# Kernel optimization log

Hardware: AMD Instinct MI355X
Metric: run time of the kernel (lower is better)

Reference implementation:

```python
import jax, jax.numpy as jnp
import numpy as np

H = 16
D_MODEL = 1024
D_K = D_MODEL // H
B, S = 4, 2048


def setup_inputs() -> dict:
    key = jax.random.key(0)
    ks = jax.random.split(key, 12)
    s = 1.0 / np.sqrt(D_MODEL)
    inp = {
        "q": jax.random.normal(ks[0], (B, S, D_MODEL), jnp.float32),
        "k": jax.random.normal(ks[1], (B, S, D_MODEL), jnp.float32),
        "v": jax.random.normal(ks[2], (B, S, D_MODEL), jnp.float32),
        "mask": jnp.ones((B, S, S), jnp.int32),
        "Wq": jax.random.normal(ks[3], (D_MODEL, D_MODEL), jnp.float32) * s,
        "bq": jnp.zeros((D_MODEL,), jnp.float32),
        "Wk": jax.random.normal(ks[4], (D_MODEL, D_MODEL), jnp.float32) * s,
        "bk": jnp.zeros((D_MODEL,), jnp.float32),
        "Wv": jax.random.normal(ks[5], (D_MODEL, D_MODEL), jnp.float32) * s,
        "bv": jnp.zeros((D_MODEL,), jnp.float32),
        "Wo": jax.random.normal(ks[6], (D_MODEL, D_MODEL), jnp.float32) * s,
        "bo": jnp.zeros((D_MODEL,), jnp.float32),
    }
    return inp


def _shape_heads(x):
    # [B, S, d_model] -> [B, H, S, d_k]
    b, s, _ = x.shape
    return x.reshape(b, s, H, D_K).transpose(0, 2, 1, 3)


def reference(q, k, v, mask, Wq, bq, Wk, bk, Wv, bv, Wo, bo):
    qh = _shape_heads(q @ Wq + bq)  # [B,H,S,dk]
    kh = _shape_heads(k @ Wk + bk)
    vh = _shape_heads(v @ Wv + bv)
    scores = jnp.einsum("bhqd,bhkd->bhqk", qh, kh) / jnp.sqrt(jnp.float32(D_K))
    scores = jnp.where(mask[:, None, :, :] == 0, jnp.float32(-1e9), scores)
    attn = jax.nn.softmax(scores, axis=-1)  # dropout = identity (eval)
    ctx = jnp.einsum("bhqk,bhkd->bhqd", attn, vh)
    concat = ctx.transpose(0, 2, 1, 3).reshape(q.shape[0], -1, D_MODEL)
    output = concat @ Wo + bo
    return output, attn
```

## Files before the change

### kernel.cpp

```cpp
#include <hip/hip_runtime.h>

#define NH     16
#define SEQ    2048
#define DMODEL 1024
#define DK     64
#define NB     4

typedef __attribute__((ext_vector_type(8))) short short8v;
typedef __attribute__((ext_vector_type(4))) short short4v;
typedef __attribute__((ext_vector_type(4))) float f32x4;

#define EXP_SC 0.18033688011f

__device__ __forceinline__ short f2bf(float x) {
  unsigned u = __float_as_uint(x);
  unsigned r = (u + 0x7FFFu + ((u >> 16) & 1u)) >> 16;
  return (short)r;
}
__device__ __forceinline__ float bf2f(short b) {
  return __uint_as_float(((unsigned)(unsigned short)b) << 16);
}

typedef const __attribute__((address_space(1))) unsigned int* gas_t;
typedef __attribute__((address_space(3))) unsigned int* las_t;
__device__ __forceinline__ void glds16(const void* g, void* l) {
  __builtin_amdgcn_global_load_lds((gas_t)g, (las_t)l, 16, 0, 0);
}

__device__ __forceinline__ void stage_tile(const void* grow0, int gpitchB,
                                           void* ltile, int wid, int lane) {
#pragma unroll
  for (int i = 0; i < 2; ++i) {
    const int row = i * 32 + wid * 8 + (lane >> 3);
    const int srccol = ((lane & 7) * 16) ^ ((lane >> 3) << 4);
    const char* src = reinterpret_cast<const char*>(grow0) + (size_t)row * gpitchB + srccol;
    char* dst = reinterpret_cast<char*>(ltile) + i * 4096 + wid * 1024;
    glds16(src, dst);
  }
}

__device__ __forceinline__ void stage_tile_h8(const void* grow0, int gpitchB,
                                              void* ltile, int wid, int lane) {
  const int row = wid * 8 + (lane >> 3);
  const int srccol = ((lane & 7) * 16) ^ ((lane >> 3) << 4);
  const char* src = reinterpret_cast<const char*>(grow0) + (size_t)row * gpitchB + srccol;
  char* dst = reinterpret_cast<char*>(ltile) + wid * 1024;
  glds16(src, dst);
}
__device__ __forceinline__ void stage_tile128(const void* grow0, int gpitchB,
                                              void* ltile, int wid, int lane) {
#pragma unroll
  for (int i = 0; i < 2; ++i) {
    const int row = i * 64 + wid * 8 + (lane >> 3);
    const int srccol = ((lane & 7) * 16) ^ ((lane >> 3) << 4);
    const char* src = reinterpret_cast<const char*>(grow0) + (size_t)row * gpitchB + srccol;
    char* dst = reinterpret_cast<char*>(ltile) + i * 8192 + wid * 1024;
    glds16(src, dst);
  }
}

__device__ __forceinline__ short8v ldfrag(const short* base, int row, int colByte) {
  return *reinterpret_cast<const short8v*>(
      reinterpret_cast<const char*>(base) + row * 128 + (colByte ^ ((row & 7) << 4)));
}
__device__ __forceinline__ void st8b(short* base, int row, int colByte, short4v v) {
  *reinterpret_cast<short4v*>(
      reinterpret_cast<char*>(base) + row * 128 + (colByte ^ ((row & 7) << 4))) = v;
}

__device__ __forceinline__ void stPf4(float* base, int row, int colByte, float4 v) {
  *reinterpret_cast<float4*>(
      reinterpret_cast<char*>(base) + row * 256 + (colByte ^ ((row & 7) << 4))) = v;
}
__device__ __forceinline__ float4 ldPf4(const float* base, int row, int colByte) {
  return *reinterpret_cast<const float4*>(
      reinterpret_cast<const char*>(base) + row * 256 + (colByte ^ ((row & 7) << 4)));
}

__global__ __launch_bounds__(256) void pack_mask_kernel(
    const int* __restrict__ mask, unsigned long long* __restrict__ bits)
{
  const int t = threadIdx.x;
  const size_t chunk = (size_t)blockIdx.x * 4 + (t >> 6);
  const int lane = t & 63;
  const int m = mask[chunk * 64 + lane];
  const unsigned long long b = __ballot(m != 0);
  if (lane == 0) bits[chunk] = b;
}

__global__ __launch_bounds__(256) void convert_f32_bf16_kernel(
    const float* __restrict__ in, short* __restrict__ out)
{
  const int idx = blockIdx.x * 256 + threadIdx.x;
  const float4 x0 = *reinterpret_cast<const float4*>(&in[(size_t)idx * 8]);
  const float4 x1 = *reinterpret_cast<const float4*>(&in[(size_t)idx * 8 + 4]);
  short8v o;
  o[0] = f2bf(x0.x); o[1] = f2bf(x0.y); o[2] = f2bf(x0.z); o[3] = f2bf(x0.w);
  o[4] = f2bf(x1.x); o[5] = f2bf(x1.y); o[6] = f2bf(x1.z); o[7] = f2bf(x1.w);
  *reinterpret_cast<short8v*>(&out[(size_t)idx * 8]) = o;
}

__global__ __launch_bounds__(256) void transpose_w_all_kernel(
    const float* __restrict__ W0, const float* __restrict__ W1,
    const float* __restrict__ W2, const float* __restrict__ W3,
    short* __restrict__ WT0, short* __restrict__ WT1,
    short* __restrict__ WT2, short* __restrict__ WT3h, short* __restrict__ WT3l)
{
  __shared__ short Th[64][80];
  __shared__ short Tl[64][80];
  const int t  = threadIdx.x;
  const int k0 = blockIdx.x * 64;
  const int n0 = blockIdx.y * 64;
  const int z  = blockIdx.z;
  const float* W = (z == 0) ? W0 : (z == 1) ? W1 : (z == 2) ? W2 : W3;

  const int kl = t >> 2, nc = (t & 3) * 16;
  if (z < 3) {
#pragma unroll
    for (int i = 0; i < 4; ++i) {
      const float4 x = *reinterpret_cast<const float4*>(&W[(size_t)(k0 + kl) * DMODEL + n0 + nc + i * 4]);
      Th[nc + i * 4 + 0][kl] = f2bf(x.x);
      Th[nc + i * 4 + 1][kl] = f2bf(x.y);
      Th[nc + i * 4 + 2][kl] = f2bf(x.z);
      Th[nc + i * 4 + 3][kl] = f2bf(x.w);
    }
    __syncthreads();
    short* WT = (z == 0) ? WT0 : (z == 1) ? WT1 : WT2;
    const int nl = t >> 2, kc = (t & 3) * 16;
#pragma unroll
    for (int i = 0; i < 2; ++i) {
      const short8v y = *reinterpret_cast<const short8v*>(&Th[nl][kc + i * 8]);
      *reinterpret_cast<short8v*>(&WT[(size_t)(n0 + nl) * DMODEL + k0 + kc + i * 8]) = y;
    }
  } else {
#pragma unroll
    for (int i = 0; i < 4; ++i) {
      const float4 x = *reinterpret_cast<const float4*>(&W[(size_t)(k0 + kl) * DMODEL + n0 + nc + i * 4]);
      const float xv[4] = {x.x, x.y, x.z, x.w};
#pragma unroll
      for (int j = 0; j < 4; ++j) {
        const short hi = f2bf(xv[j]);
        const short lo = f2bf(xv[j] - bf2f(hi));
        Th[nc + i * 4 + j][kl] = hi;
        Tl[nc + i * 4 + j][kl] = lo;
      }
    }
    __syncthreads();
    const int nl = t >> 2, kc = (t & 3) * 16;
#pragma unroll
    for (int i = 0; i < 2; ++i) {
      const short8v yh = *reinterpret_cast<const short8v*>(&Th[nl][kc + i * 8]);
      const short8v yl = *reinterpret_cast<const short8v*>(&Tl[nl][kc + i * 8]);
      *reinterpret_cast<short8v*>(&WT3h[(size_t)(n0 + nl) * DMODEL + k0 + kc + i * 8]) = yh;
      *reinterpret_cast<short8v*>(&WT3l[(size_t)(n0 + nl) * DMODEL + k0 + kc + i * 8]) = yl;
    }
  }
}

__global__ __launch_bounds__(256) void proj_mfma_kernel(
    const short* __restrict__ A,
    const short* __restrict__ BT,
    const float* __restrict__ bias,
    short* __restrict__ out)
{
  __shared__ short As[128 * 64];
  __shared__ short Bs[128 * 64];

  const int t = threadIdx.x, lane = t & 63, wid = t >> 6;
  const int g = lane >> 4, r15 = lane & 15;
  const int lid = (blockIdx.x & 7) * 64 + (blockIdx.x >> 3);
  const int m0 = (lid >> 3) * 128, n0 = (lid & 7) * 128;
  const int wm = (wid >> 1) * 64, wn = (wid & 1) * 64;

  f32x4 acc[4][4];
#pragma unroll
  for (int i = 0; i < 4; ++i)
#pragma unroll
    for (int j = 0; j < 4; ++j) acc[i][j] = (f32x4){0.f, 0.f, 0.f, 0.f};

  for (int k0 = 0; k0 < DMODEL; k0 += 64) {
    __syncthreads();
    stage_tile(A + (size_t)m0 * DMODEL + k0, DMODEL * 2, As, wid, lane);
    stage_tile(A + (size_t)(m0 + 64) * DMODEL + k0, DMODEL * 2, As + 64 * 64, wid, lane);
    stage_tile(BT + (size_t)n0 * DMODEL + k0, DMODEL * 2, Bs, wid, lane);
    stage_tile(BT + (size_t)(n0 + 64) * DMODEL + k0, DMODEL * 2, Bs + 64 * 64, wid, lane);
    __syncthreads();

#pragma unroll
    for (int w = 0; w < 2; ++w) {
      short8v a[4], b[4];
#pragma unroll
      for (int i = 0; i < 4; ++i) a[i] = ldfrag(As, wm + i * 16 + r15, w * 64 + g * 16);
#pragma unroll
      for (int j = 0; j < 4; ++j) b[j] = ldfrag(Bs, wn + j * 16 + r15, w * 64 + g * 16);
#pragma unroll
      for (int i = 0; i < 4; ++i)
#pragma unroll
        for (int j = 0; j < 4; ++j)
          acc[i][j] = __builtin_amdgcn_mfma_f32_16x16x32_bf16(a[i], b[j], acc[i][j], 0, 0, 0);
    }
  }

#pragma unroll
  for (int j = 0; j < 4; ++j) {
    const int n = n0 + wn + j * 16 + r15;
    const int hh = n >> 6, dd = n & 63;
    const float bv = bias[n];
#pragma unroll
    for (int i = 0; i < 4; ++i) {
#pragma unroll
      for (int reg = 0; reg < 4; ++reg) {
        const int m = m0 + wm + i * 16 + g * 4 + reg;
        const int bb = m >> 11, ss = m & 2047;
        out[((size_t)(bb * NH + hh) * SEQ + ss) * DK + dd] = f2bf(acc[i][j][reg] + bv);
      }
    }
  }
}

__global__ __launch_bounds__(256) void outproj_mfma_kernel(
    const short* __restrict__ Ahp, const short* __restrict__ Alp,
    const short* __restrict__ BTh, const short* __restrict__ BTl,
    const float* __restrict__ bias, float* __restrict__ out)
{
  __shared__ short Ah[128 * 64];
  __shared__ short Al[128 * 64];
  __shared__ short Bh[128 * 64];
  __shared__ short Bl[128 * 64];

  const int t = threadIdx.x, lane = t & 63, wid = t >> 6;
  const int g = lane >> 4, r15 = lane & 15;
  const int lid = (blockIdx.x & 7) * 64 + (blockIdx.x >> 3);
  const int m0 = (lid >> 3) * 128, n0 = (lid & 7) * 128;
  const int wm = (wid >> 1) * 64, wn = (wid & 1) * 64;

  f32x4 acc[4][4];
#pragma unroll
  for (int i = 0; i < 4; ++i)
#pragma unroll
    for (int j = 0; j < 4; ++j) acc[i][j] = (f32x4){0.f, 0.f, 0.f, 0.f};

  for (int k0 = 0; k0 < DMODEL; k0 += 64) {
    __syncthreads();
    stage_tile(Ahp + (size_t)m0 * DMODEL + k0, DMODEL * 2, Ah, wid, lane);
    stage_tile(Ahp + (size_t)(m0 + 64) * DMODEL + k0, DMODEL * 2, Ah + 64 * 64, wid, lane);
    stage_tile(Alp + (size_t)m0 * DMODEL + k0, DMODEL * 2, Al, wid, lane);
    stage_tile(Alp + (size_t)(m0 + 64) * DMODEL + k0, DMODEL * 2, Al + 64 * 64, wid, lane);
    stage_tile(BTh + (size_t)n0 * DMODEL + k0, DMODEL * 2, Bh, wid, lane);
    stage_tile(BTh + (size_t)(n0 + 64) * DMODEL + k0, DMODEL * 2, Bh + 64 * 64, wid, lane);
    stage_tile(BTl + (size_t)n0 * DMODEL + k0, DMODEL * 2, Bl, wid, lane);
    stage_tile(BTl + (size_t)(n0 + 64) * DMODEL + k0, DMODEL * 2, Bl + 64 * 64, wid, lane);
    __syncthreads();

#pragma unroll
    for (int w = 0; w < 2; ++w) {
      short8v ah[4], al[4];
#pragma unroll
      for (int i = 0; i < 4; ++i) {
        ah[i] = ldfrag(Ah, wm + i * 16 + r15, w * 64 + g * 16);
        al[i] = ldfrag(Al, wm + i * 16 + r15, w * 64 + g * 16);
      }
#pragma unroll
      for (int j = 0; j < 4; ++j) {
        const short8v bh = ldfrag(Bh, wn + j * 16 + r15, w * 64 + g * 16);
        const short8v bl = ldfrag(Bl, wn + j * 16 + r15, w * 64 + g * 16);
#pragma unroll
        for (int i = 0; i < 4; ++i) {
          acc[i][j] = __builtin_amdgcn_mfma_f32_16x16x32_bf16(ah[i], bh, acc[i][j], 0, 0, 0);
          acc[i][j] = __builtin_amdgcn_mfma_f32_16x16x32_bf16(ah[i], bl, acc[i][j], 0, 0, 0);
          acc[i][j] = __builtin_amdgcn_mfma_f32_16x16x32_bf16(al[i], bh, acc[i][j], 0, 0, 0);
        }
      }
    }
  }

#pragma unroll
  for (int j = 0; j < 4; ++j) {
    const int n = n0 + wn + j * 16 + r15;
    const float bv = bias[n];
#pragma unroll
    for (int i = 0; i < 4; ++i)
#pragma unroll
      for (int reg = 0; reg < 4; ++reg) {
        const int m = m0 + wm + i * 16 + g * 4 + reg;
        out[(size_t)m * DMODEL + n] = acc[i][j][reg] + bv;
      }
  }
}

__global__ __launch_bounds__(256) void transpose_v_kernel(
    const short* __restrict__ vhb, short* __restrict__ vT)
{
  __shared__ short T[64][72];
  const int t    = threadIdx.x;
  const int s0   = blockIdx.x * 64;
  const int head = blockIdx.y;
  const size_t ibase = (size_t)head * SEQ * DK;
  const size_t obase = (size_t)head * DK * SEQ;

  const int sl = t >> 2, d0 = (t & 3) * 16;
#pragma unroll
  for (int i = 0; i < 2; ++i) {
    const short8v x = *reinterpret_cast<const short8v*>(
        &vhb[ibase + (size_t)(s0 + sl) * DK + d0 + i * 8]);
#pragma unroll
    for (int j = 0; j < 8; ++j) T[d0 + i * 8 + j][sl] = x[j];
  }
  __syncthreads();
  const int dl = t >> 2, soff = (t & 3) * 16;
#pragma unroll
  for (int i = 0; i < 2; ++i) {
    const short8v y = *reinterpret_cast<const short8v*>(&T[dl][soff + i * 8]);
    *reinterpret_cast<short8v*>(&vT[obase + (size_t)dl * SEQ + s0 + soff + i * 8]) = y;
  }
}

__global__ __launch_bounds__(512) void flash_kernel(
    const short* __restrict__ qh, const short* __restrict__ kh,
    const short* __restrict__ vT, const unsigned long long* __restrict__ maskbits,
    short* __restrict__ ctxh, short* __restrict__ ctxl,
    float* __restrict__ linv_arr)
{
  __shared__ short Qs[128 * 64];
  __shared__ short Ks[2][64 * 64];
  __shared__ short VsT[2][64 * 64];
  __shared__ short Psb[128 * 64];

  const int t    = threadIdx.x;
  const int lane = t & 63;
  const int wid  = t >> 6;
  const int g    = lane >> 4;
  const int r15  = lane & 15;
  const int qbase = wid * 16;
  const int qrow  = qbase + r15;

  const int bid = blockIdx.x;
  const int swz = (bid & 7) * 128 + (bid >> 3);
  const int qt = swz & 15;
  const int h  = (swz >> 4) & 15;
  const int b  = swz >> 8;
  const int q0 = qt * 128;

  const size_t headbase = ((size_t)(b * NH + h)) * SEQ * DK;
  const size_t vTbase   = ((size_t)(b * NH + h)) * DK * SEQ;
  const size_t mrow     = ((size_t)b * SEQ + (q0 + qrow)) * (SEQ / 64);

  stage_tile128(qh + headbase + (size_t)q0 * DK, DK * 2, Qs, wid, lane);
  stage_tile_h8(kh + headbase, DK * 2, Ks[0], wid, lane);
  stage_tile_h8(reinterpret_cast<const char*>(vT + vTbase), SEQ * 2, VsT[0], wid, lane);
  asm volatile("s_waitcnt vmcnt(0)" ::: "memory");
  __builtin_amdgcn_s_barrier();

  const short8v bQ0 = ldfrag(Qs, qrow, g * 16);
  const short8v bQ1 = ldfrag(Qs, qrow, 64 + g * 16);

  float lsum = 0.f;
  f32x4 cacc[4];
#pragma unroll
  for (int i = 0; i < 4; ++i) cacc[i] = (f32x4){0.f, 0.f, 0.f, 0.f};

  for (int t64 = 0; t64 < 32; ++t64) {
    const int cur = t64 & 1;
    if (t64 < 31) {
      stage_tile_h8(kh + headbase + (size_t)(t64 + 1) * 64 * DK, DK * 2,
                    Ks[cur ^ 1], wid, lane);
      stage_tile_h8(reinterpret_cast<const char*>(vT + vTbase + (t64 + 1) * 64), SEQ * 2,
                    VsT[cur ^ 1], wid, lane);
    }
    __builtin_amdgcn_sched_barrier(0);

    f32x4 acc[4];
#pragma unroll
    for (int t4 = 0; t4 < 4; ++t4) acc[t4] = (f32x4){0.f, 0.f, 0.f, 0.f};
#pragma unroll
    for (int t4 = 0; t4 < 4; ++t4) {
      const short8v aK0 = ldfrag(Ks[cur], t4 * 16 + r15, g * 16);
      const short8v aK1 = ldfrag(Ks[cur], t4 * 16 + r15, 64 + g * 16);
      acc[t4] = __builtin_amdgcn_mfma_f32_16x16x32_bf16(aK0, bQ0, acc[t4], 0, 0, 0);
      acc[t4] = __builtin_amdgcn_mfma_f32_16x16x32_bf16(aK1, bQ1, acc[t4], 0, 0, 0);
    }

    const unsigned long long mb = maskbits[mrow + t64];
    if (__all(mb == ~0ULL)) {
#pragma unroll
      for (int t4 = 0; t4 < 4; ++t4) {
        short4v pk;
#pragma unroll
        for (int reg = 0; reg < 4; ++reg) {
          const float p = exp2f(acc[t4][reg] * EXP_SC);
          lsum += p;
          pk[reg] = f2bf(p);
        }
        st8b(Psb, qrow, t4 * 32 + g * 8, pk);
      }
    } else {
#pragma unroll
      for (int t4 = 0; t4 < 4; ++t4) {
        const unsigned b4 = (unsigned)(mb >> (t4 * 16 + g * 4)) & 0xFu;
        short4v pk;
#pragma unroll
        for (int reg = 0; reg < 4; ++reg) {
          const float p = ((b4 >> reg) & 1u) ? exp2f(acc[t4][reg] * EXP_SC) : 0.f;
          lsum += p;
          pk[reg] = f2bf(p);
        }
        st8b(Psb, qrow, t4 * 32 + g * 8, pk);
      }
    }

    {
      const short8v aP0 = ldfrag(Psb, qrow, g * 16);
      const short8v aP1 = ldfrag(Psb, qrow, 64 + g * 16);
#pragma unroll
      for (int dt = 0; dt < 4; ++dt) {
        const short8v bV0 = ldfrag(VsT[cur], dt * 16 + r15, g * 16);
        const short8v bV1 = ldfrag(VsT[cur], dt * 16 + r15, 64 + g * 16);
        cacc[dt] = __builtin_amdgcn_mfma_f32_16x16x32_bf16(aP0, bV0, cacc[dt], 0, 0, 0);
        cacc[dt] = __builtin_amdgcn_mfma_f32_16x16x32_bf16(aP1, bV1, cacc[dt], 0, 0, 0);
      }
    }

    asm volatile("s_waitcnt vmcnt(0)" ::: "memory");
    __builtin_amdgcn_s_barrier();
  }

  float l = lsum;
  l += __shfl_xor(l, 16);
  l += __shfl_xor(l, 32);
  const float linv = 1.0f / l;
  if (g == 0)
    linv_arr[(size_t)(b * NH + h) * SEQ + q0 + qrow] = linv;

  float linvr[4];
#pragma unroll
  for (int reg = 0; reg < 4; ++reg) linvr[reg] = __shfl(linv, g * 4 + reg);

#pragma unroll
  for (int dt = 0; dt < 4; ++dt)
#pragma unroll
    for (int reg = 0; reg < 4; ++reg) {
      const float x = cacc[dt][reg] * linvr[reg];
      const short hi = f2bf(x);
      const short lo = f2bf(x - bf2f(hi));
      const size_t off = (size_t)(b * SEQ + q0 + qbase + g * 4 + reg) * DMODEL
                       + h * DK + dt * 16 + r15;
      ctxh[off] = hi;
      ctxl[off] = lo;
    }
}

__global__ __launch_bounds__(512) void probs_kernel(
    const short* __restrict__ qh, const short* __restrict__ kh,
    const unsigned long long* __restrict__ maskbits,
    const float* __restrict__ linv_arr,
    float* __restrict__ attn_out)
{
  __shared__ short Qs[128 * 64];
  __shared__ short Ks[2][64 * 64];
  __shared__ float PsbF[128 * 64];

  const int t    = threadIdx.x;
  const int lane = t & 63;
  const int wid  = t >> 6;
  const int g    = lane >> 4;
  const int r15  = lane & 15;
  const int qbase = wid * 16;
  const int qrow  = qbase + r15;

  const int bid = blockIdx.x;
  const int swz = (bid & 7) * 128 + (bid >> 3);
  const int qt = swz & 15;
  const int h  = (swz >> 4) & 15;
  const int b  = swz >> 8;
  const int q0 = qt * 128;

  const size_t headbase = ((size_t)(b * NH + h)) * SEQ * DK;
  const size_t attnbase = ((size_t)(b * NH + h)) * SEQ * SEQ;
  const size_t mrow     = ((size_t)b * SEQ + (q0 + qrow)) * (SEQ / 64);

  const float linv  = linv_arr[(size_t)(b * NH + h) * SEQ + q0 + qrow];
  const float llinv = log2f(linv);

  stage_tile128(qh + headbase + (size_t)q0 * DK, DK * 2, Qs, wid, lane);
  stage_tile_h8(kh + headbase, DK * 2, Ks[0], wid, lane);
  asm volatile("s_waitcnt vmcnt(0)" ::: "memory");
  __builtin_amdgcn_s_barrier();

  const short8v bQ0 = ldfrag(Qs, qrow, g * 16);
  const short8v bQ1 = ldfrag(Qs, qrow, 64 + g * 16);

  for (int t64 = 0; t64 < 32; ++t64) {
    const int cur = t64 & 1;
    if (t64 + 1 < 32)
      stage_tile_h8(kh + headbase + (size_t)(t64 + 1) * 64 * DK, DK * 2,
                    Ks[cur ^ 1], wid, lane);
    __builtin_amdgcn_sched_barrier(0);

    f32x4 acc[4];
#pragma unroll
    for (int t4 = 0; t4 < 4; ++t4) acc[t4] = (f32x4){0.f, 0.f, 0.f, 0.f};
#pragma unroll
    for (int t4 = 0; t4 < 4; ++t4) {
      const short8v aK0 = ldfrag(Ks[cur], t4 * 16 + r15, g * 16);
      const short8v aK1 = ldfrag(Ks[cur], t4 * 16 + r15, 64 + g * 16);
      acc[t4] = __builtin_amdgcn_mfma_f32_16x16x32_bf16(aK0, bQ0, acc[t4], 0, 0, 0);
      acc[t4] = __builtin_amdgcn_mfma_f32_16x16x32_bf16(aK1, bQ1, acc[t4], 0, 0, 0);
    }

    const unsigned long long mb = maskbits[mrow + t64];
    if (__all(mb == ~0ULL)) {
#pragma unroll
      for (int t4 = 0; t4 < 4; ++t4) {
        float4 pv;
        pv.x = exp2f(fmaf(acc[t4][0], EXP_SC, llinv));
        pv.y = exp2f(fmaf(acc[t4][1], EXP_SC, llinv));
        pv.z = exp2f(fmaf(acc[t4][2], EXP_SC, llinv));
        pv.w = exp2f(fmaf(acc[t4][3], EXP_SC, llinv));
        stPf4(PsbF, qrow, t4 * 64 + g * 16, pv);
      }
    } else {
#pragma unroll
      for (int t4 = 0; t4 < 4; ++t4) {
        const unsigned b4 = (unsigned)(mb >> (t4 * 16 + g * 4)) & 0xFu;
        float4 pv;
        pv.x = (b4 & 1u) ? exp2f(acc[t4][0] * EXP_SC) * linv : 0.f;
        pv.y = (b4 & 2u) ? exp2f(acc[t4][1] * EXP_SC) * linv : 0.f;
        pv.z = (b4 & 4u) ? exp2f(acc[t4][2] * EXP_SC) * linv : 0.f;
        pv.w = (b4 & 8u) ? exp2f(acc[t4][3] * EXP_SC) * linv : 0.f;
        stPf4(PsbF, qrow, t4 * 64 + g * 16, pv);
      }
    }

#pragma unroll
    for (int i = 0; i < 4; ++i) {
      const int prow = qbase + i * 4 + g;
      const float4 f = ldPf4(PsbF, prow, r15 * 16);
      f32x4 fv; fv[0] = f.x; fv[1] = f.y; fv[2] = f.z; fv[3] = f.w;
      __builtin_nontemporal_store(fv, reinterpret_cast<f32x4*>(
          &attn_out[attnbase + (size_t)(q0 + prow) * SEQ + t64 * 64 + r15 * 4]));
    }

    asm volatile("s_waitcnt vmcnt(4)" ::: "memory");
    __builtin_amdgcn_s_barrier();
  }
}


extern "C" void kernel_launch(void* const* d_in, const int* in_sizes, int n_in,
                              void* d_out, int out_size, void* d_ws, size_t ws_size,
                              hipStream_t stream) {
  const float* q    = (const float*)d_in[0];
  const float* k    = (const float*)d_in[1];
  const float* v    = (const float*)d_in[2];
  const int*   mask = (const int*)d_in[3];
  const float* Wq   = (const float*)d_in[4];
  const float* bq   = (const float*)d_in[5];
  const float* Wk   = (const float*)d_in[6];
  const float* bk   = (const float*)d_in[7];
  const float* Wv   = (const float*)d_in[8];
  const float* bv   = (const float*)d_in[9];
  const float* Wo   = (const float*)d_in[10];
  const float* bo   = (const float*)d_in[11];

  float* out  = (float*)d_out;
  float* attn = out + (size_t)NB * SEQ * DMODEL;

  const size_t HSZ = (size_t)NB * NH * SEQ * DK;
  const size_t WSZ = (size_t)DMODEL * DMODEL;
  short* qhb  = (short*)d_ws;
  short* khb  = qhb + HSZ;
  short* vhb  = khb + HSZ;
  short* Xbuf = vhb + HSZ;
  short* vTb  = Xbuf + HSZ;
  short* WTq  = vTb + HSZ;
  short* WTk  = WTq + WSZ;
  short* WTv  = WTk + WSZ;
  short* WToh = WTv + WSZ;
  short* WTol = WToh + WSZ;
  unsigned long long* maskbits = (unsigned long long*)(WTol + WSZ);
  float* linv_arr = (float*)(maskbits + (size_t)NB * SEQ * (SEQ / 64));
  short* ctxh = vhb;
  short* ctxl = Xbuf;

  const dim3 blk(256);
  const dim3 blk8(512);

  pack_mask_kernel<<<dim3((NB * SEQ * SEQ / 64) / 4), blk, 0, stream>>>(mask, maskbits);

  transpose_w_all_kernel<<<dim3(16, 16, 4), blk, 0, stream>>>(
      Wq, Wk, Wv, Wo, WTq, WTk, WTv, WToh, WTol);

  const int nconv = (int)(NB * SEQ * DMODEL / 8 / 256);
  const int ngemm = 512;

  convert_f32_bf16_kernel<<<nconv, blk, 0, stream>>>(q, Xbuf);
  proj_mfma_kernel<<<ngemm, blk, 0, stream>>>(Xbuf, WTq, bq, qhb);
  convert_f32_bf16_kernel<<<nconv, blk, 0, stream>>>(k, Xbuf);
  proj_mfma_kernel<<<ngemm, blk, 0, stream>>>(Xbuf, WTk, bk, khb);
  convert_f32_bf16_kernel<<<nconv, blk, 0, stream>>>(v, Xbuf);
  proj_mfma_kernel<<<ngemm, blk, 0, stream>>>(Xbuf, WTv, bv, vhb);

  transpose_v_kernel<<<dim3(SEQ / 64, NB * NH), blk, 0, stream>>>(vhb, vTb);

  const int nattn = (SEQ / 128) * NH * NB;
  flash_kernel<<<nattn, blk8, 0, stream>>>(qhb, khb, vTb, maskbits,
                                           ctxh, ctxl, linv_arr);
  probs_kernel<<<nattn, blk8, 0, stream>>>(qhb, khb, maskbits, linv_arr, attn);

  outproj_mfma_kernel<<<ngemm, blk, 0, stream>>>(ctxh, ctxl, WToh, WTol, bo, out);
}
```

Baseline: 520.8 us.

## Fuse fp32-to-bf16 conversion into QKV projection and batch three projections in one launch

```diff
diff --git a/kernel.cpp b/kernel.cpp
--- a/kernel.cpp
+++ b/kernel.cpp
@@ -36,6 +36,23 @@
     const char* src = reinterpret_cast<const char*>(grow0) + (size_t)row * gpitchB + srccol;
     char* dst = reinterpret_cast<char*>(ltile) + i * 4096 + wid * 1024;
     glds16(src, dst);
+  }
+}
+
+__device__ __forceinline__ void stage_tile_cvt(const float* grow0, int gpitchF,
+                                               short* ltile, int wid, int lane) {
+#pragma unroll
+  for (int i = 0; i < 2; ++i) {
+    const int row = i * 32 + wid * 8 + (lane >> 3);
+    const float* src = grow0 + (size_t)row * gpitchF + (lane & 7) * 8;
+    const float4 x0 = *reinterpret_cast<const float4*>(src);
+    const float4 x1 = *reinterpret_cast<const float4*>(src + 4);
+    short8v o;
+    o[0] = f2bf(x0.x); o[1] = f2bf(x0.y); o[2] = f2bf(x0.z); o[3] = f2bf(x0.w);
+    o[4] = f2bf(x1.x); o[5] = f2bf(x1.y); o[6] = f2bf(x1.z); o[7] = f2bf(x1.w);
+    char* dst = reinterpret_cast<char*>(ltile) + row * 128
+              + (((lane & 7) * 16) ^ ((row & 7) << 4));
+    *reinterpret_cast<short8v*>(dst) = o;
   }
 }
 
@@ -86,18 +103,6 @@
   const int m = mask[chunk * 64 + lane];
   const unsigned long long b = __ballot(m != 0);
   if (lane == 0) bits[chunk] = b;
-}
-
-__global__ __launch_bounds__(256) void convert_f32_bf16_kernel(
-    const float* __restrict__ in, short* __restrict__ out)
-{
-  const int idx = blockIdx.x * 256 + threadIdx.x;
-  const float4 x0 = *reinterpret_cast<const float4*>(&in[(size_t)idx * 8]);
-  const float4 x1 = *reinterpret_cast<const float4*>(&in[(size_t)idx * 8 + 4]);
-  short8v o;
-  o[0] = f2bf(x0.x); o[1] = f2bf(x0.y); o[2] = f2bf(x0.z); o[3] = f2bf(x0.w);
-  o[4] = f2bf(x1.x); o[5] = f2bf(x1.y); o[6] = f2bf(x1.z); o[7] = f2bf(x1.w);
-  *reinterpret_cast<short8v*>(&out[(size_t)idx * 8]) = o;
 }
 
 __global__ __launch_bounds__(256) void transpose_w_all_kernel(
@@ -157,21 +162,31 @@
   }
 }
 
-__global__ __launch_bounds__(256) void proj_mfma_kernel(
-    const short* __restrict__ A,
-    const short* __restrict__ BT,
-    const float* __restrict__ bias,
-    short* __restrict__ out)
+__global__ __launch_bounds__(256) void proj3_mfma_kernel(
+    const float* __restrict__ Xq, const float* __restrict__ Xk,
+    const float* __restrict__ Xv,
+    const short* __restrict__ WTq, const short* __restrict__ WTk,
+    const short* __restrict__ WTv,
+    const float* __restrict__ bq, const float* __restrict__ bk,
+    const float* __restrict__ bv,
+    short* __restrict__ oq, short* __restrict__ ok, short* __restrict__ ov)
 {
   __shared__ short As[128 * 64];
   __shared__ short Bs[128 * 64];
 
   const int t = threadIdx.x, lane = t & 63, wid = t >> 6;
   const int g = lane >> 4, r15 = lane & 15;
-  const int lid = (blockIdx.x & 7) * 64 + (blockIdx.x >> 3);
+  const int lid3 = (blockIdx.x & 7) * 192 + (blockIdx.x >> 3);
+  const int p   = lid3 >> 9;
+  const int lid = lid3 & 511;
   const int m0 = (lid >> 3) * 128, n0 = (lid & 7) * 128;
   const int wm = (wid >> 1) * 64, wn = (wid & 1) * 64;
 
+  const float* A  = (p == 0) ? Xq : (p == 1) ? Xk : Xv;
+  const short* BT = (p == 0) ? WTq : (p == 1) ? WTk : WTv;
+  const float* bias = (p == 0) ? bq : (p == 1) ? bk : bv;
+  short* out = (p == 0) ? oq : (p == 1) ? ok : ov;
+
   f32x4 acc[4][4];
 #pragma unroll
   for (int i = 0; i < 4; ++i)
@@ -180,8 +195,8 @@
 
   for (int k0 = 0; k0 < DMODEL; k0 += 64) {
     __syncthreads();
-    stage_tile(A + (size_t)m0 * DMODEL + k0, DMODEL * 2, As, wid, lane);
-    stage_tile(A + (size_t)(m0 + 64) * DMODEL + k0, DMODEL * 2, As + 64 * 64, wid, lane);
+    stage_tile_cvt(A + (size_t)m0 * DMODEL + k0, DMODEL, As, wid, lane);
+    stage_tile_cvt(A + (size_t)(m0 + 64) * DMODEL + k0, DMODEL, As + 64 * 64, wid, lane);
     stage_tile(BT + (size_t)n0 * DMODEL + k0, DMODEL * 2, Bs, wid, lane);
     stage_tile(BT + (size_t)(n0 + 64) * DMODEL + k0, DMODEL * 2, Bs + 64 * 64, wid, lane);
     __syncthreads();
@@ -205,14 +220,14 @@
   for (int j = 0; j < 4; ++j) {
     const int n = n0 + wn + j * 16 + r15;
     const int hh = n >> 6, dd = n & 63;
-    const float bv = bias[n];
+    const float bv_ = bias[n];
 #pragma unroll
     for (int i = 0; i < 4; ++i) {
 #pragma unroll
       for (int reg = 0; reg < 4; ++reg) {
         const int m = m0 + wm + i * 16 + g * 4 + reg;
         const int bb = m >> 11, ss = m & 2047;
-        out[((size_t)(bb * NH + hh) * SEQ + ss) * DK + dd] = f2bf(acc[i][j][reg] + bv);
+        out[((size_t)(bb * NH + hh) * SEQ + ss) * DK + dd] = f2bf(acc[i][j][reg] + bv_);
       }
     }
   }
@@ -590,15 +605,8 @@
   transpose_w_all_kernel<<<dim3(16, 16, 4), blk, 0, stream>>>(
       Wq, Wk, Wv, Wo, WTq, WTk, WTv, WToh, WTol);
 
-  const int nconv = (int)(NB * SEQ * DMODEL / 8 / 256);
-  const int ngemm = 512;
-
-  convert_f32_bf16_kernel<<<nconv, blk, 0, stream>>>(q, Xbuf);
-  proj_mfma_kernel<<<ngemm, blk, 0, stream>>>(Xbuf, WTq, bq, qhb);
-  convert_f32_bf16_kernel<<<nconv, blk, 0, stream>>>(k, Xbuf);
-  proj_mfma_kernel<<<ngemm, blk, 0, stream>>>(Xbuf, WTk, bk, khb);
-  convert_f32_bf16_kernel<<<nconv, blk, 0, stream>>>(v, Xbuf);
-  proj_mfma_kernel<<<ngemm, blk, 0, stream>>>(Xbuf, WTv, bv, vhb);
+  proj3_mfma_kernel<<<1536, blk, 0, stream>>>(
+      q, k, v, WTq, WTk, WTv, bq, bk, bv, qhb, khb, vhb);
 
   transpose_v_kernel<<<dim3(SEQ / 64, NB * NH), blk, 0, stream>>>(vhb, vTb);
 
@@ -607,5 +615,6 @@
                                            ctxh, ctxl, linv_arr);
   probs_kernel<<<nattn, blk8, 0, stream>>>(qhb, khb, maskbits, linv_arr, attn);
 
+  const int ngemm = 512;
   outproj_mfma_kernel<<<ngemm, blk, 0, stream>>>(ctxh, ctxl, WToh, WTol, bo, out);
 }
```

Measured after the change: 534.6 us. 1.03x slower.
